# Performance work log

Hardware: AMD Instinct MI355X
Metric: run time of the kernel (lower is better)

The kernel has to match this reference:

```python
import jax, jax.numpy as jnp
import numpy as np

EPS = 1e-3  # BatchNormalization epsilon


def setup_inputs() -> dict:
    key = jax.random.key(0)
    ks = jax.random.split(key, 8)
    B, H, W, C = 16, 128, 128, 128
    f = C // 2  # filters = max(1, C // 2)
    x = jax.random.normal(ks[0], (B, H, W, C), dtype=jnp.float32)
    s_in = 1.0 / np.sqrt(C)
    s_f = 1.0 / np.sqrt(f)
    return {
        "x": x,
        "Wg": jax.random.normal(ks[1], (C, f), dtype=jnp.float32) * s_in,
        "bg": jnp.zeros((f,), jnp.float32),
        "Wt": jax.random.normal(ks[2], (C, f), dtype=jnp.float32) * s_in,
        "bt": jnp.zeros((f,), jnp.float32),
        "Wp": jax.random.normal(ks[3], (C, f), dtype=jnp.float32) * s_in,
        "bp": jnp.zeros((f,), jnp.float32),
        "Wo": jax.random.normal(ks[4], (f, f), dtype=jnp.float32) * s_f,
        "bo": jnp.zeros((f,), jnp.float32),
        "gamma": jnp.ones((f,), jnp.float32),
        "beta": jnp.zeros((f,), jnp.float32),
        "moving_mean": jnp.zeros((f,), jnp.float32),
        "moving_var": jnp.ones((f,), jnp.float32),
    }


def reference(x, Wg, bg, Wt, bt, Wp, bp, Wo, bo, gamma, beta, moving_mean, moving_var):
    B, H, W, C = x.shape
    f = Wg.shape[1]
    N = H * W
    # 1x1 conv projections (NHWC): einsum over channel dim, then flatten spatial
    g = (jnp.einsum('bhwc,cf->bhwf', x, Wg) + bg).reshape(B, N, f)     # [B,N,f]
    tx = (jnp.einsum('bhwc,cf->bhwf', x, Wt) + bt).reshape(B, N, f)    # theta
    ty = (jnp.einsum('bhwc,cf->bhwf', x, Wp) + bp).reshape(B, N, f)    # phi
    # keras Dot(axes=[1,2]) on ([B,N,f], Permute->[B,f,N]) contracts the N axes
    # -> f x f Gram matrix per batch element.
    fm = jnp.einsum('bni,bnj->bij', tx, ty)                            # [B,f,f]
    fm = jax.nn.softmax(fm, axis=-1)
    # second Dot(axes=[1,2]): contract fm axis 1 (i) with g axis 2 (i) -> [B,f,N]
    z = jnp.einsum('bij,bni->bjn', fm, g)                              # [B,f,N]
    # Reshape flat-reinterprets [B, f*N] as [B,H,W,f]
    z = z.reshape(B, H, W, f)
    # output 1x1 conv (f -> f channels)
    z = jnp.einsum('bhwf,fe->bhwe', z, Wo) + bo
    # BatchNorm, inference mode (moving statistics)
    inv = gamma * jax.lax.rsqrt(moving_var + EPS)
    z = (z - moving_mean) * inv + beta
    return z
```

## Files before the change

kernel.cpp:

```cpp
#include <hip/hip_runtime.h>
#include <stdint.h>

#define B_ 16
#define H_ 128
#define W_ 128
#define C_ 128
#define F_ 64
#define N_ (H_*W_)
#define SPLITS 32
#define RPB (N_/SPLITS)
#define CH 64
#define EPSV 1e-3f

typedef __attribute__((ext_vector_type(8))) short bf16x8;
typedef __attribute__((ext_vector_type(16))) float f32x16;

__device__ __forceinline__ unsigned short f2b(float f) {
    unsigned int x = __float_as_uint(f);
    x += 0x7fffu + ((x >> 16) & 1u);
    return (unsigned short)(x >> 16);
}
__device__ __forceinline__ float b2f(unsigned short u) {
    return __uint_as_float(((unsigned int)u) << 16);
}

__global__ __launch_bounds__(256, 2)
void kS(const float* __restrict__ x, const float* __restrict__ Wg,
        const float* __restrict__ bg, unsigned short* __restrict__ g,
        float* __restrict__ Spart, float* __restrict__ cspart)
{
    __shared__ unsigned int  xsT_hi[C_][36];
    __shared__ unsigned int  xsT_lo[C_][36];
    __shared__ __align__(16) unsigned short xs_pool[CH][136];
    __shared__ __align__(16) unsigned short gT[CH][72];

    const int tid  = threadIdx.x;
    const int lane = tid & 63;
    const int w    = tid >> 6;
    const int b    = blockIdx.x >> 5;
    const int sp   = blockIdx.x & 31;

    const float* xb = x + ((size_t)b * N_ + (size_t)sp * RPB) * C_;
    unsigned short* gb = g + ((size_t)b * N_ + (size_t)sp * RPB) * F_;

    const int rowA = lane & 31;
    const int hiL  = lane >> 5;
    const int kgrp = hiL * 8;
    const int c1b  = (w & 1) * 64;
    const int c2b  = (w >> 1) * 64;
    const int nbG  = (w & 1) * 32;
    const int fbG  = (w >> 1) * 32;

    const float bgl = bg[fbG + rowA];

    for (int i = tid; i < C_*F_; i += 256) {
        int c = i >> 6, f = i & 63;
        xs_pool[f][c] = f2b(Wg[i]);
    }
    __syncthreads();
    bf16x8 wgfr[8];
    #pragma unroll
    for (int ks = 0; ks < 8; ++ks)
        wgfr[ks] = *(const bf16x8*)&xs_pool[fbG + rowA][ks*16 + kgrp];
    __syncthreads();

    f32x16 accS[2][2];
    #pragma unroll
    for (int ti = 0; ti < 2; ++ti)
        #pragma unroll
        for (int tj = 0; tj < 2; ++tj)
            #pragma unroll
            for (int e = 0; e < 16; ++e) accS[ti][tj][e] = 0.f;
    float csum = 0.f;

    const int sr = tid >> 2;
    const int sc = (tid & 3) * 16;

    for (int ch = 0; ch < RPB/CH; ++ch) {
        const float* xc = xb + (size_t)ch * CH * C_;
        #pragma unroll
        for (int p = 0; p < 4; ++p) {
            const int idx = tid + 256*p;
            const int np  = idx & 31;
            const int c4  = (idx >> 5) * 4;
            const float* r0 = xc + (size_t)(2*np) * C_ + c4;
            float4 a = *(const float4*)r0;
            float4 q = *(const float4*)(r0 + C_);
            unsigned short ha0 = f2b(a.x), ha1 = f2b(a.y), ha2 = f2b(a.z), ha3 = f2b(a.w);
            unsigned short hb0 = f2b(q.x), hb1 = f2b(q.y), hb2 = f2b(q.z), hb3 = f2b(q.w);
            unsigned short la0 = f2b(a.x - b2f(ha0)), la1 = f2b(a.y - b2f(ha1));
            unsigned short la2 = f2b(a.z - b2f(ha2)), la3 = f2b(a.w - b2f(ha3));
            unsigned short lb0 = f2b(q.x - b2f(hb0)), lb1 = f2b(q.y - b2f(hb1));
            unsigned short lb2 = f2b(q.z - b2f(hb2)), lb3 = f2b(q.w - b2f(hb3));
            if (p == 0) __syncthreads();
            xsT_hi[c4+0][np] = (unsigned)ha0 | ((unsigned)hb0 << 16);
            xsT_hi[c4+1][np] = (unsigned)ha1 | ((unsigned)hb1 << 16);
            xsT_hi[c4+2][np] = (unsigned)ha2 | ((unsigned)hb2 << 16);
            xsT_hi[c4+3][np] = (unsigned)ha3 | ((unsigned)hb3 << 16);
            xsT_lo[c4+0][np] = (unsigned)la0 | ((unsigned)lb0 << 16);
            xsT_lo[c4+1][np] = (unsigned)la1 | ((unsigned)lb1 << 16);
            xsT_lo[c4+2][np] = (unsigned)la2 | ((unsigned)lb2 << 16);
            xsT_lo[c4+3][np] = (unsigned)la3 | ((unsigned)lb3 << 16);
            ushort4 u0; u0.x = ha0; u0.y = ha1; u0.z = ha2; u0.w = ha3;
            ushort4 u1; u1.x = hb0; u1.y = hb1; u1.z = hb2; u1.w = hb3;
            *(ushort4*)&xs_pool[2*np  ][c4] = u0;
            *(ushort4*)&xs_pool[2*np+1][c4] = u1;
        }

        if (ch) {
            uint4 v0 = *(const uint4*)&gT[sr][sc];
            uint4 v1 = *(const uint4*)&gT[sr][sc + 8];
            unsigned short* dst = gb + (size_t)((ch-1)*CH + sr) * F_ + sc;
            *(uint4*)dst       = v0;
            *(uint4*)(dst + 8) = v1;
        }
        __syncthreads();

        if (tid < C_) {
            #pragma unroll 8
            for (int npp = 0; npp < 32; ++npp) {
                unsigned int h = xsT_hi[tid][npp];
                unsigned int l = xsT_lo[tid][npp];
                csum += b2f((unsigned short)(h & 0xffffu)) + b2f((unsigned short)(h >> 16))
                      + b2f((unsigned short)(l & 0xffffu)) + b2f((unsigned short)(l >> 16));
            }
        }

        {
            f32x16 aG;
            #pragma unroll
            for (int e = 0; e < 16; ++e) aG[e] = 0.f;
            #pragma unroll
            for (int ks = 0; ks < 8; ++ks) {
                bf16x8 av = *(const bf16x8*)&xs_pool[nbG + rowA][ks*16 + kgrp];
                aG = __builtin_amdgcn_mfma_f32_32x32x16_bf16(av, wgfr[ks], aG, 0, 0, 0);
            }
            const int fcol = fbG + rowA;
            #pragma unroll
            for (int r = 0; r < 16; ++r) {
                int nloc = (r & 3) + 8*(r >> 2) + 4*hiL;
                gT[nbG + nloc][fcol] = f2b(aG[r] + bgl);
            }
        }

        #pragma unroll
        for (int ks = 0; ks < 4; ++ks) {
            const int kn = ks*16 + kgrp;
            bf16x8 Ah[2], Al[2], Bh[2], Bl[2];
            #pragma unroll
            for (int t = 0; t < 2; ++t) {
                const unsigned short* rAh = (const unsigned short*)&xsT_hi[c1b + 32*t + rowA][0];
                const unsigned short* rAl = (const unsigned short*)&xsT_lo[c1b + 32*t + rowA][0];
                Ah[t] = *(const bf16x8*)(rAh + kn);
                Al[t] = *(const bf16x8*)(rAl + kn);
                const unsigned short* rBh = (const unsigned short*)&xsT_hi[c2b + 32*t + rowA][0];
                const unsigned short* rBl = (const unsigned short*)&xsT_lo[c2b + 32*t + rowA][0];
                Bh[t] = *(const bf16x8*)(rBh + kn);
                Bl[t] = *(const bf16x8*)(rBl + kn);
            }
            #pragma unroll
            for (int ti = 0; ti < 2; ++ti)
                #pragma unroll
                for (int tj = 0; tj < 2; ++tj) {
                    accS[ti][tj] = __builtin_amdgcn_mfma_f32_32x32x16_bf16(Ah[ti], Bh[tj], accS[ti][tj], 0, 0, 0);
                    accS[ti][tj] = __builtin_amdgcn_mfma_f32_32x32x16_bf16(Ah[ti], Bl[tj], accS[ti][tj], 0, 0, 0);
                    accS[ti][tj] = __builtin_amdgcn_mfma_f32_32x32x16_bf16(Al[ti], Bh[tj], accS[ti][tj], 0, 0, 0);
                }
        }
    }

    __syncthreads();
    {
        uint4 v0 = *(const uint4*)&gT[sr][sc];
        uint4 v1 = *(const uint4*)&gT[sr][sc + 8];
        unsigned short* dst = gb + (size_t)((RPB/CH - 1)*CH + sr) * F_ + sc;
        *(uint4*)dst       = v0;
        *(uint4*)(dst + 8) = v1;
    }

    float* so = Spart + (size_t)(b * SPLITS + sp) * (size_t)(C_ * C_);
    #pragma unroll
    for (int ti = 0; ti < 2; ++ti)
        #pragma unroll
        for (int tj = 0; tj < 2; ++tj)
            #pragma unroll
            for (int r = 0; r < 16; ++r) {
                int c1 = c1b + 32*ti + (r & 3) + 8*(r >> 2) + 4*hiL;
                int c2 = c2b + 32*tj + rowA;
                so[(size_t)c1 * C_ + c2] = accS[ti][tj][r];
            }
    if (tid < C_)
        cspart[(size_t)(b * SPLITS + sp) * C_ + tid] = csum;
}

__global__ __launch_bounds__(256, 8)
void kR(const float* __restrict__ Spart, const float* __restrict__ cspart,
        float* __restrict__ Sred, float* __restrict__ csred)
{
    const int b = blockIdx.x >> 4;
    const int r = blockIdx.x & 15;
    const int f4 = r*256 + threadIdx.x;
    const float4* base = (const float4*)(Spart + (size_t)b * SPLITS * C_ * C_);
    float sx=0.f, sy=0.f, sz=0.f, sw=0.f;
    #pragma unroll 4
    for (int sp = 0; sp < SPLITS; ++sp) {
        float4 v = base[(size_t)sp * (C_*C_/4) + f4];
        sx += v.x; sy += v.y; sz += v.z; sw += v.w;
    }
    ((float4*)(Sred + (size_t)b * C_ * C_))[f4] = make_float4(sx, sy, sz, sw);

    if (r == 0 && threadIdx.x < C_) {
        float c = 0.f;
        #pragma unroll 4
        for (int sp = 0; sp < SPLITS; ++sp)
            c += cspart[((size_t)b * SPLITS + sp) * C_ + threadIdx.x];
        csred[(size_t)b * C_ + threadIdx.x] = c;
    }
}

__global__ __launch_bounds__(256, 2)
void kT(const float* __restrict__ Sred, const float* __restrict__ csred,
        const float* __restrict__ Wp, float* __restrict__ T1buf,
        float* __restrict__ T2buf)
{
    __shared__ float Ss[32][C_];
    __shared__ float Wps[C_][F_];

    const int tid = threadIdx.x;
    const int b = blockIdx.x >> 2;
    const int q = blockIdx.x & 3;

    const float4* sg = (const float4*)(Sred + ((size_t)b * C_ + q*32) * C_);
    for (int t = tid; t < 32*C_/4; t += 256) ((float4*)Ss)[t] = sg[t];
    const float4* wg = (const float4*)Wp;
    for (int t = tid; t < C_*F_/4; t += 256) ((float4*)Wps)[t] = wg[t];
    __syncthreads();

    const int lane = tid & 63;
    const int w    = tid >> 6;

    float acc[8] = {0.f,0.f,0.f,0.f,0.f,0.f,0.f,0.f};
    #pragma unroll 2
    for (int k = 0; k < C_; k += 4) {
        float w0 = Wps[k+0][lane];
        float w1 = Wps[k+1][lane];
        float w2 = Wps[k+2][lane];
        float w3 = Wps[k+3][lane];
        #pragma unroll
        for (int cl = 0; cl < 8; ++cl) {
            float4 sv = *(const float4*)&Ss[w*8 + cl][k];
            float t = acc[cl];
            t = fmaf(sv.x, w0, t);
            t = fmaf(sv.y, w1, t);
            t = fmaf(sv.z, w2, t);
            t = fmaf(sv.w, w3, t);
            acc[cl] = t;
        }
    }
    #pragma unroll
    for (int cl = 0; cl < 8; ++cl) {
        int c = q*32 + w*8 + cl;
        T1buf[((size_t)b * C_ + c) * F_ + lane] = acc[cl];
    }

    if (q == 0 && tid < F_) {
        const float* cv = csred + (size_t)b * C_;
        float s = 0.f;
        for (int k = 0; k < C_; ++k) s = fmaf(cv[k], Wps[k][tid], s);
        T2buf[(size_t)b * F_ + tid] = s;
    }
}

__global__ __launch_bounds__(256, 2)
void kF(const float* __restrict__ T1buf, const float* __restrict__ T2buf,
        const float* __restrict__ csred, const float* __restrict__ Wt,
        const float* __restrict__ bt, const float* __restrict__ bp,
        float* __restrict__ U)
{
    __shared__ float T1s[C_][F_];
    __shared__ float Wts[C_][F_];
    __shared__ float csb[C_];
    __shared__ float T2s[F_], T3s[F_], bts[F_], bps[F_];

    const int tid = threadIdx.x;
    const int b = blockIdx.x;

    for (int t = tid; t < C_*F_/4; t += 256) {
        ((float4*)T1s)[t] = ((const float4*)(T1buf + (size_t)b * C_ * F_))[t];
        ((float4*)Wts)[t] = ((const float4*)Wt)[t];
    }
    if (tid < C_) csb[tid] = csred[(size_t)b * C_ + tid];
    if (tid < F_) {
        T2s[tid] = T2buf[(size_t)b * F_ + tid];
        bts[tid] = bt[tid];
        bps[tid] = bp[tid];
    }
    __syncthreads();

    if (tid < F_) {
        float s = 0.f;
        for (int c = 0; c < C_; ++c) s = fmaf(csb[c], Wts[c][tid], s);
        T3s[tid] = s;
    }
    __syncthreads();

    const int lane = tid & 63;
    const int w    = tid >> 6;

    float acc[16];
    #pragma unroll
    for (int r = 0; r < 16; ++r) acc[r] = 0.f;

    #pragma unroll 2
    for (int c = 0; c < C_; ++c) {
        float t1 = T1s[c][lane];
        #pragma unroll
        for (int u = 0; u < 4; ++u) {
            float4 wv = *(const float4*)&Wts[c][w*16 + u*4];
            acc[u*4+0] = fmaf(wv.x, t1, acc[u*4+0]);
            acc[u*4+1] = fmaf(wv.y, t1, acc[u*4+1]);
            acc[u*4+2] = fmaf(wv.z, t1, acc[u*4+2]);
            acc[u*4+3] = fmaf(wv.w, t1, acc[u*4+3]);
        }
    }

    const float bpj = bps[lane];
    const float t2j = T2s[lane];
    #pragma unroll
    for (int r = 0; r < 16; ++r) {
        const int i = w*16 + r;
        float v = acc[r] + T3s[i]*bpj + bts[i]*(t2j + (float)N_ * bpj);
        float m = v;
        #pragma unroll
        for (int o = 32; o; o >>= 1) m = fmaxf(m, __shfl_xor(m, o));
        float e = expf(v - m);
        float s = e;
        #pragma unroll
        for (int o = 32; o; o >>= 1) s += __shfl_xor(s, o);
        U[((size_t)b * F_ + i) * F_ + lane] = e / s;
    }
}

__global__ __launch_bounds__(256, 2)
void kC(const unsigned short* __restrict__ g, const float* __restrict__ U,
        const float* __restrict__ Wo, const float* __restrict__ bo,
        const float* __restrict__ gamma_, const float* __restrict__ beta_,
        const float* __restrict__ mmean, const float* __restrict__ mvar,
        float* __restrict__ out)
{
    __shared__ __align__(16) unsigned short UT[F_][72];
    __shared__ __align__(16) unsigned short WoT[F_][72];
    __shared__ __align__(16) unsigned short M1T[4][32][72];

    const int tid  = threadIdx.x;
    const int lane = tid & 63;
    const int wv   = tid >> 6;
    const int jt   = wv & 1;
    const int et   = wv >> 1;

    const int wgrp = blockIdx.x & 15;
    const int half = (blockIdx.x >> 4) & 1;
    const int b    = blockIdx.x >> 5;

    for (int t = tid; t < 1024; t += 256) {
        const int i  = t >> 4;
        const int j4 = (t & 15) * 4;
        float4 uv = *(const float4*)(U + ((size_t)b * F_ + i) * F_ + j4);
        UT[j4+0][i] = f2b(uv.x); UT[j4+1][i] = f2b(uv.y);
        UT[j4+2][i] = f2b(uv.z); UT[j4+3][i] = f2b(uv.w);
        float4 wo4 = *(const float4*)(Wo + (size_t)i * F_ + j4);
        WoT[j4+0][i] = f2b(wo4.x); WoT[j4+1][i] = f2b(wo4.y);
        WoT[j4+2][i] = f2b(wo4.z); WoT[j4+3][i] = f2b(wo4.w);
    }
    __syncthreads();

    const int rowA = lane & 31;
    const int hi   = lane >> 5;
    const int hi8  = hi * 8;

    bf16x8 Ufr[4], WoFr[4];
    #pragma unroll
    for (int ks = 0; ks < 4; ++ks) {
        Ufr[ks]  = *(const bf16x8*)&UT [32*jt + rowA][16*ks + hi8];
        WoFr[ks] = *(const bf16x8*)&WoT[32*et + rowA][16*ks + hi8];
    }

    const int ep = 32*et + rowA;
    const float scl = gamma_[ep] * rsqrtf(mvar[ep] + EPSV);
    const float sft = (bo[ep] - mmean[ep]) * scl + beta_[ep];

    const unsigned short* gB = g + ((size_t)b * N_ + (size_t)half * (N_/2)) * F_;
    float* outB = out + (((size_t)b * H_ + half) * W_) * F_ + ep;
    const int w0 = wgrp * 8;

    unsigned short* m1row = &M1T[wv][rowA][0];

    auto gload = [&](bf16x8 (&D)[2][4], int widx) {
        const unsigned short* gw = gB + (size_t)widx * (64*F_) + (size_t)rowA * F_ + hi8;
        #pragma unroll
        for (int ft = 0; ft < 2; ++ft)
            #pragma unroll
            for (int ks = 0; ks < 4; ++ks)
                D[ft][ks] = *(const bf16x8*)(gw + ft*(32*F_) + 16*ks);
    };

    auto body = [&](bf16x8 (&G)[2][4], int widx) {
        f32x16 m0, m1, a2r;
        #pragma unroll
        for (int e = 0; e < 16; ++e) { m0[e] = 0.f; m1[e] = 0.f; a2r[e] = 0.f; }
        #pragma unroll
        for (int ks = 0; ks < 4; ++ks) {
            m0 = __builtin_amdgcn_mfma_f32_32x32x16_bf16(G[0][ks], Ufr[ks], m0, 0, 0, 0);
            m1 = __builtin_amdgcn_mfma_f32_32x32x16_bf16(G[1][ks], Ufr[ks], m1, 0, 0, 0);
        }
        #pragma unroll
        for (int r = 0; r < 16; r += 2) {
            const int e0 = (r & 3) + 8*(r >> 2) + 4*hi;
            const unsigned pw0 = (unsigned)f2b(m0[r]) | ((unsigned)f2b(m0[r+1]) << 16);
            *(unsigned int*)(m1row + e0) = pw0;
            const unsigned pw1 = (unsigned)f2b(m1[r]) | ((unsigned)f2b(m1[r+1]) << 16);
            *(unsigned int*)(m1row + 32 + e0) = pw1;
        }
        __syncthreads();
        #pragma unroll
        for (int ksg = 0; ksg < 4; ++ksg) {
            bf16x8 af = *(const bf16x8*)(m1row + 16*ksg + hi8);
            a2r = __builtin_amdgcn_mfma_f32_32x32x16_bf16(af, WoFr[ksg], a2r, 0, 0, 0);
        }
        float* ow = outB + (size_t)widx * F_ + (size_t)(64*jt + 8*hi) * (W_*F_);
        #pragma unroll
        for (int r = 0; r < 16; ++r) {
            const int off2j = 2*(r & 3) + 16*(r >> 2);
            ow[(size_t)off2j * (W_*F_)] = a2r[r] * scl + sft;
        }
        __syncthreads();
    };

    bf16x8 GA[2][4], GBf[2][4];
    gload(GA, w0);
    #pragma unroll
    for (int wi = 0; wi < 8; ++wi) {
        if (wi & 1) {
            if (wi < 7) gload(GA, w0 + wi + 1);
            body(GBf, w0 + wi);
        } else {
            if (wi < 7) gload(GBf, w0 + wi + 1);
            body(GA, w0 + wi);
        }
    }
}

extern "C" void kernel_launch(void* const* d_in, const int* in_sizes, int n_in,
                              void* d_out, int out_size, void* d_ws, size_t ws_size,
                              hipStream_t stream)
{
    const float* x  = (const float*)d_in[0];
    const float* Wg = (const float*)d_in[1];
    const float* bg = (const float*)d_in[2];
    const float* Wt = (const float*)d_in[3];
    const float* bt = (const float*)d_in[4];
    const float* Wp = (const float*)d_in[5];
    const float* bp = (const float*)d_in[6];
    const float* Wo = (const float*)d_in[7];
    const float* bo = (const float*)d_in[8];
    const float* ga = (const float*)d_in[9];
    const float* be = (const float*)d_in[10];
    const float* mm = (const float*)d_in[11];
    const float* mv = (const float*)d_in[12];
    float* out = (float*)d_out;

    char* ws = (char*)d_ws;
    unsigned short* g = (unsigned short*)ws;
    size_t off = (size_t)B_ * N_ * F_ * sizeof(unsigned short);
    float* Spart = (float*)(ws + off);
    float* T1buf = (float*)(ws + off);
    off += (size_t)B_ * SPLITS * C_ * C_ * sizeof(float);
    float* cspart = (float*)(ws + off);
    off += (size_t)B_ * SPLITS * C_ * sizeof(float);
    float* U = (float*)(ws + off);
    off += (size_t)B_ * F_ * F_ * sizeof(float);
    float* Sred = (float*)(ws + off);
    off += (size_t)B_ * C_ * C_ * sizeof(float);
    float* csred = (float*)(ws + off);
    off += (size_t)B_ * C_ * sizeof(float);
    float* T2buf = (float*)(ws + off);

    kS<<<B_ * SPLITS, 256, 0, stream>>>(x, Wg, bg, g, Spart, cspart);
    kR<<<B_ * 16, 256, 0, stream>>>(Spart, cspart, Sred, csred);
    kT<<<B_ * 4, 256, 0, stream>>>(Sred, csred, Wp, T1buf, T2buf);
    kF<<<B_, 256, 0, stream>>>(T1buf, T2buf, csred, Wt, bt, bp, U);
    kC<<<B_ * 2 * (W_/8), 256, 0, stream>>>(g, U, Wo, bo, ga, be, mm, mv, out);
}
```

Measured before the change: 110.2 us.

## Double kS block to 512 threads and split Gram tiles across eight waves

```diff
diff --git a/kernel.cpp b/kernel.cpp
--- a/kernel.cpp
+++ b/kernel.cpp
@@ -24,7 +24,7 @@
     return __uint_as_float(((unsigned int)u) << 16);
 }
 
-__global__ __launch_bounds__(256, 2)
+__global__ __launch_bounds__(512, 2)
 void kS(const float* __restrict__ x, const float* __restrict__ Wg,
         const float* __restrict__ bg, unsigned short* __restrict__ g,
         float* __restrict__ Spart, float* __restrict__ cspart)
@@ -36,7 +36,7 @@
 
     const int tid  = threadIdx.x;
     const int lane = tid & 63;
-    const int w    = tid >> 6;
+    const int v    = tid >> 6;
     const int b    = blockIdx.x >> 5;
     const int sp   = blockIdx.x & 31;
 
@@ -46,41 +46,40 @@
     const int rowA = lane & 31;
     const int hiL  = lane >> 5;
     const int kgrp = hiL * 8;
-    const int c1b  = (w & 1) * 64;
-    const int c2b  = (w >> 1) * 64;
-    const int nbG  = (w & 1) * 32;
-    const int fbG  = (w >> 1) * 32;
-
-    const float bgl = bg[fbG + rowA];
-
-    for (int i = tid; i < C_*F_; i += 256) {
+    const int rb   = v >> 1;
+    const int cbB  = (v & 1) * 64;
+    const int nbG  = (v & 1) * 32;
+    const int fbG  = (v >> 1) * 32;
+
+    const float bgl = (v < 4) ? bg[fbG + rowA] : 0.f;
+
+    for (int i = tid; i < C_*F_; i += 512) {
         int c = i >> 6, f = i & 63;
         xs_pool[f][c] = f2b(Wg[i]);
     }
     __syncthreads();
     bf16x8 wgfr[8];
-    #pragma unroll
-    for (int ks = 0; ks < 8; ++ks)
-        wgfr[ks] = *(const bf16x8*)&xs_pool[fbG + rowA][ks*16 + kgrp];
-    __syncthreads();
-
-    f32x16 accS[2][2];
-    #pragma unroll
-    for (int ti = 0; ti < 2; ++ti)
-        #pragma unroll
-        for (int tj = 0; tj < 2; ++tj)
-            #pragma unroll
-            for (int e = 0; e < 16; ++e) accS[ti][tj][e] = 0.f;
+    if (v < 4) {
+        #pragma unroll
+        for (int ks = 0; ks < 8; ++ks)
+            wgfr[ks] = *(const bf16x8*)&xs_pool[fbG + rowA][ks*16 + kgrp];
+    }
+
+    f32x16 accS[2];
+    #pragma unroll
+    for (int t = 0; t < 2; ++t)
+        #pragma unroll
+        for (int e = 0; e < 16; ++e) accS[t][e] = 0.f;
     float csum = 0.f;
 
-    const int sr = tid >> 2;
-    const int sc = (tid & 3) * 16;
+    const int sr = tid >> 3;
+    const int sc = (tid & 7) * 8;
 
     for (int ch = 0; ch < RPB/CH; ++ch) {
         const float* xc = xb + (size_t)ch * CH * C_;
         #pragma unroll
-        for (int p = 0; p < 4; ++p) {
-            const int idx = tid + 256*p;
+        for (int p = 0; p < 2; ++p) {
+            const int idx = tid + 512*p;
             const int np  = idx & 31;
             const int c4  = (idx >> 5) * 4;
             const float* r0 = xc + (size_t)(2*np) * C_ + c4;
@@ -107,26 +106,26 @@
             *(ushort4*)&xs_pool[2*np+1][c4] = u1;
         }
 
+        uint4 gv;
+        if (ch) gv = *(const uint4*)&gT[sr][sc];
+        __syncthreads();
         if (ch) {
-            uint4 v0 = *(const uint4*)&gT[sr][sc];
-            uint4 v1 = *(const uint4*)&gT[sr][sc + 8];
             unsigned short* dst = gb + (size_t)((ch-1)*CH + sr) * F_ + sc;
-            *(uint4*)dst       = v0;
-            *(uint4*)(dst + 8) = v1;
-        }
-        __syncthreads();
-
-        if (tid < C_) {
+            *(uint4*)dst = gv;
+        }
+
+        if (tid >= 256 && tid < 384) {
+            const int c = tid - 256;
             #pragma unroll 8
             for (int npp = 0; npp < 32; ++npp) {
-                unsigned int h = xsT_hi[tid][npp];
-                unsigned int l = xsT_lo[tid][npp];
+                unsigned int h = xsT_hi[c][npp];
+                unsigned int l = xsT_lo[c][npp];
                 csum += b2f((unsigned short)(h & 0xffffu)) + b2f((unsigned short)(h >> 16))
                       + b2f((unsigned short)(l & 0xffffu)) + b2f((unsigned short)(l >> 16));
             }
         }
 
-        {
+        if (v < 4) {
             f32x16 aG;
             #pragma unroll
             for (int e = 0; e < 16; ++e) aG[e] = 0.f;
@@ -146,51 +145,41 @@
         #pragma unroll
         for (int ks = 0; ks < 4; ++ks) {
             const int kn = ks*16 + kgrp;
-            bf16x8 Ah[2], Al[2], Bh[2], Bl[2];
+            bf16x8 Ah, Al, Bh[2], Bl[2];
+            Ah = *(const bf16x8*)((const unsigned short*)&xsT_hi[rb*32 + rowA][0] + kn);
+            Al = *(const bf16x8*)((const unsigned short*)&xsT_lo[rb*32 + rowA][0] + kn);
             #pragma unroll
             for (int t = 0; t < 2; ++t) {
-                const unsigned short* rAh = (const unsigned short*)&xsT_hi[c1b + 32*t + rowA][0];
-                const unsigned short* rAl = (const unsigned short*)&xsT_lo[c1b + 32*t + rowA][0];
-                Ah[t] = *(const bf16x8*)(rAh + kn);
-                Al[t] = *(const bf16x8*)(rAl + kn);
-                const unsigned short* rBh = (const unsigned short*)&xsT_hi[c2b + 32*t + rowA][0];
-                const unsigned short* rBl = (const unsigned short*)&xsT_lo[c2b + 32*t + rowA][0];
-                Bh[t] = *(const bf16x8*)(rBh + kn);
-                Bl[t] = *(const bf16x8*)(rBl + kn);
+                Bh[t] = *(const bf16x8*)((const unsigned short*)&xsT_hi[cbB + 32*t + rowA][0] + kn);
+                Bl[t] = *(const bf16x8*)((const unsigned short*)&xsT_lo[cbB + 32*t + rowA][0] + kn);
             }
             #pragma unroll
-            for (int ti = 0; ti < 2; ++ti)
-                #pragma unroll
-                for (int tj = 0; tj < 2; ++tj) {
-                    accS[ti][tj] = __builtin_amdgcn_mfma_f32_32x32x16_bf16(Ah[ti], Bh[tj], accS[ti][tj], 0, 0, 0);
-                    accS[ti][tj] = __builtin_amdgcn_mfma_f32_32x32x16_bf16(Ah[ti], Bl[tj], accS[ti][tj], 0, 0, 0);
-                    accS[ti][tj] = __builtin_amdgcn_mfma_f32_32x32x16_bf16(Al[ti], Bh[tj], accS[ti][tj], 0, 0, 0);
-                }
+            for (int t = 0; t < 2; ++t) {
+                accS[t] = __builtin_amdgcn_mfma_f32_32x32x16_bf16(Ah, Bh[t], accS[t], 0, 0, 0);
+                accS[t] = __builtin_amdgcn_mfma_f32_32x32x16_bf16(Ah, Bl[t], accS[t], 0, 0, 0);
+                accS[t] = __builtin_amdgcn_mfma_f32_32x32x16_bf16(Al, Bh[t], accS[t], 0, 0, 0);
+            }
         }
     }
 
     __syncthreads();
     {
-        uint4 v0 = *(const uint4*)&gT[sr][sc];
-        uint4 v1 = *(const uint4*)&gT[sr][sc + 8];
+        uint4 gv = *(const uint4*)&gT[sr][sc];
         unsigned short* dst = gb + (size_t)((RPB/CH - 1)*CH + sr) * F_ + sc;
-        *(uint4*)dst       = v0;
-        *(uint4*)(dst + 8) = v1;
+        *(uint4*)dst = gv;
     }
 
     float* so = Spart + (size_t)(b * SPLITS + sp) * (size_t)(C_ * C_);
     #pragma unroll
-    for (int ti = 0; ti < 2; ++ti)
-        #pragma unroll
-        for (int tj = 0; tj < 2; ++tj)
-            #pragma unroll
-            for (int r = 0; r < 16; ++r) {
-                int c1 = c1b + 32*ti + (r & 3) + 8*(r >> 2) + 4*hiL;
-                int c2 = c2b + 32*tj + rowA;
-                so[(size_t)c1 * C_ + c2] = accS[ti][tj][r];
-            }
-    if (tid < C_)
-        cspart[(size_t)(b * SPLITS + sp) * C_ + tid] = csum;
+    for (int t = 0; t < 2; ++t)
+        #pragma unroll
+        for (int r = 0; r < 16; ++r) {
+            int c1 = rb*32 + (r & 3) + 8*(r >> 2) + 4*hiL;
+            int c2 = cbB + 32*t + rowA;
+            so[(size_t)c1 * C_ + c2] = accS[t][r];
+        }
+    if (tid >= 256 && tid < 384)
+        cspart[(size_t)(b * SPLITS + sp) * C_ + (tid - 256)] = csum;
 }
 
 __global__ __launch_bounds__(256, 8)
@@ -485,7 +474,7 @@
     off += (size_t)B_ * C_ * sizeof(float);
     float* T2buf = (float*)(ws + off);
 
-    kS<<<B_ * SPLITS, 256, 0, stream>>>(x, Wg, bg, g, Spart, cspart);
+    kS<<<B_ * SPLITS, 512, 0, stream>>>(x, Wg, bg, g, Spart, cspart);
     kR<<<B_ * 16, 256, 0, stream>>>(Spart, cspart, Sred, csred);
     kT<<<B_ * 4, 256, 0, stream>>>(Sred, csred, Wp, T1buf, T2buf);
     kF<<<B_, 256, 0, stream>>>(T1buf, T2buf, csred, Wt, bt, bp, U);
```

Measured after the change: 133.1 us. +20.9%, slower.

## Double-buffer shared memory in kS and prefetch next x chunk into registers

Applied to the files above, without the earlier changes.

```diff
diff --git a/kernel.cpp b/kernel.cpp
--- a/kernel.cpp
+++ b/kernel.cpp
@@ -10,6 +10,7 @@
 #define SPLITS 32
 #define RPB (N_/SPLITS)
 #define CH 64
+#define NCH (RPB/CH)
 #define EPSV 1e-3f
 
 typedef __attribute__((ext_vector_type(8))) short bf16x8;
@@ -24,15 +25,15 @@
     return __uint_as_float(((unsigned int)u) << 16);
 }
 
-__global__ __launch_bounds__(256, 2)
+__global__ __launch_bounds__(256, 1)
 void kS(const float* __restrict__ x, const float* __restrict__ Wg,
         const float* __restrict__ bg, unsigned short* __restrict__ g,
         float* __restrict__ Spart, float* __restrict__ cspart)
 {
-    __shared__ unsigned int  xsT_hi[C_][36];
-    __shared__ unsigned int  xsT_lo[C_][36];
-    __shared__ __align__(16) unsigned short xs_pool[CH][136];
-    __shared__ __align__(16) unsigned short gT[CH][72];
+    __shared__ unsigned int  xsT_hi[2][C_][36];
+    __shared__ unsigned int  xsT_lo[2][C_][36];
+    __shared__ __align__(16) unsigned short xs_pool[2][CH][136];
+    __shared__ __align__(16) unsigned short gT[2][CH][72];
 
     const int tid  = threadIdx.x;
     const int lane = tid & 63;
@@ -55,13 +56,13 @@
 
     for (int i = tid; i < C_*F_; i += 256) {
         int c = i >> 6, f = i & 63;
-        xs_pool[f][c] = f2b(Wg[i]);
+        xs_pool[0][f][c] = f2b(Wg[i]);
     }
     __syncthreads();
     bf16x8 wgfr[8];
     #pragma unroll
     for (int ks = 0; ks < 8; ++ks)
-        wgfr[ks] = *(const bf16x8*)&xs_pool[fbG + rowA][ks*16 + kgrp];
+        wgfr[ks] = *(const bf16x8*)&xs_pool[0][fbG + rowA][ks*16 + kgrp];
     __syncthreads();
 
     f32x16 accS[2][2];
@@ -76,7 +77,9 @@
     const int sr = tid >> 2;
     const int sc = (tid & 3) * 16;
 
-    for (int ch = 0; ch < RPB/CH; ++ch) {
+    float4 ra[4], rq[4];
+
+    auto loadChunk = [&](int ch) {
         const float* xc = xb + (size_t)ch * CH * C_;
         #pragma unroll
         for (int p = 0; p < 4; ++p) {
@@ -84,77 +87,81 @@
             const int np  = idx & 31;
             const int c4  = (idx >> 5) * 4;
             const float* r0 = xc + (size_t)(2*np) * C_ + c4;
-            float4 a = *(const float4*)r0;
-            float4 q = *(const float4*)(r0 + C_);
+            ra[p] = *(const float4*)r0;
+            rq[p] = *(const float4*)(r0 + C_);
+        }
+    };
+
+    auto convertStore = [&](int par) {
+        #pragma unroll
+        for (int p = 0; p < 4; ++p) {
+            const int idx = tid + 256*p;
+            const int np  = idx & 31;
+            const int c4  = (idx >> 5) * 4;
+            float4 a = ra[p], q = rq[p];
             unsigned short ha0 = f2b(a.x), ha1 = f2b(a.y), ha2 = f2b(a.z), ha3 = f2b(a.w);
             unsigned short hb0 = f2b(q.x), hb1 = f2b(q.y), hb2 = f2b(q.z), hb3 = f2b(q.w);
             unsigned short la0 = f2b(a.x - b2f(ha0)), la1 = f2b(a.y - b2f(ha1));
             unsigned short la2 = f2b(a.z - b2f(ha2)), la3 = f2b(a.w - b2f(ha3));
             unsigned short lb0 = f2b(q.x - b2f(hb0)), lb1 = f2b(q.y - b2f(hb1));
             unsigned short lb2 = f2b(q.z - b2f(hb2)), lb3 = f2b(q.w - b2f(hb3));
-            if (p == 0) __syncthreads();
-            xsT_hi[c4+0][np] = (unsigned)ha0 | ((unsigned)hb0 << 16);
-            xsT_hi[c4+1][np] = (unsigned)ha1 | ((unsigned)hb1 << 16);
-            xsT_hi[c4+2][np] = (unsigned)ha2 | ((unsigned)hb2 << 16);
-            xsT_hi[c4+3][np] = (unsigned)ha3 | ((unsigned)hb3 << 16);
-            xsT_lo[c4+0][np] = (unsigned)la0 | ((unsigned)lb0 << 16);
-            xsT_lo[c4+1][np] = (unsigned)la1 | ((unsigned)lb1 << 16);
-            xsT_lo[c4+2][np] = (unsigned)la2 | ((unsigned)lb2 << 16);
-            xsT_lo[c4+3][np] = (unsigned)la3 | ((unsigned)lb3 << 16);
+            xsT_hi[par][c4+0][np] = (unsigned)ha0 | ((unsigned)hb0 << 16);
+            xsT_hi[par][c4+1][np] = (unsigned)ha1 | ((unsigned)hb1 << 16);
+            xsT_hi[par][c4+2][np] = (unsigned)ha2 | ((unsigned)hb2 << 16);
+            xsT_hi[par][c4+3][np] = (unsigned)ha3 | ((unsigned)hb3 << 16);
+            xsT_lo[par][c4+0][np] = (unsigned)la0 | ((unsigned)lb0 << 16);
+            xsT_lo[par][c4+1][np] = (unsigned)la1 | ((unsigned)lb1 << 16);
+            xsT_lo[par][c4+2][np] = (unsigned)la2 | ((unsigned)lb2 << 16);
+            xsT_lo[par][c4+3][np] = (unsigned)la3 | ((unsigned)lb3 << 16);
             ushort4 u0; u0.x = ha0; u0.y = ha1; u0.z = ha2; u0.w = ha3;
             ushort4 u1; u1.x = hb0; u1.y = hb1; u1.z = hb2; u1.w = hb3;
-            *(ushort4*)&xs_pool[2*np  ][c4] = u0;
-            *(ushort4*)&xs_pool[2*np+1][c4] = u1;
-        }
-
-        if (ch) {
-            uint4 v0 = *(const uint4*)&gT[sr][sc];
-            uint4 v1 = *(const uint4*)&gT[sr][sc + 8];
-            unsigned short* dst = gb + (size_t)((ch-1)*CH + sr) * F_ + sc;
-            *(uint4*)dst       = v0;
-            *(uint4*)(dst + 8) = v1;
-        }
-        __syncthreads();
-
+            *(ushort4*)&xs_pool[par][2*np  ][c4] = u0;
+            *(ushort4*)&xs_pool[par][2*np+1][c4] = u1;
+        }
+    };
+
+    auto csumPhase = [&](int par) {
         if (tid < C_) {
             #pragma unroll 8
             for (int npp = 0; npp < 32; ++npp) {
-                unsigned int h = xsT_hi[tid][npp];
-                unsigned int l = xsT_lo[tid][npp];
+                unsigned int h = xsT_hi[par][tid][npp];
+                unsigned int l = xsT_lo[par][tid][npp];
                 csum += b2f((unsigned short)(h & 0xffffu)) + b2f((unsigned short)(h >> 16))
                       + b2f((unsigned short)(l & 0xffffu)) + b2f((unsigned short)(l >> 16));
             }
         }
-
-        {
-            f32x16 aG;
-            #pragma unroll
-            for (int e = 0; e < 16; ++e) aG[e] = 0.f;
-            #pragma unroll
-            for (int ks = 0; ks < 8; ++ks) {
-                bf16x8 av = *(const bf16x8*)&xs_pool[nbG + rowA][ks*16 + kgrp];
-                aG = __builtin_amdgcn_mfma_f32_32x32x16_bf16(av, wgfr[ks], aG, 0, 0, 0);
-            }
-            const int fcol = fbG + rowA;
-            #pragma unroll
-            for (int r = 0; r < 16; ++r) {
-                int nloc = (r & 3) + 8*(r >> 2) + 4*hiL;
-                gT[nbG + nloc][fcol] = f2b(aG[r] + bgl);
-            }
-        }
-
+    };
+
+    auto gPhase = [&](int par) {
+        f32x16 aG;
+        #pragma unroll
+        for (int e = 0; e < 16; ++e) aG[e] = 0.f;
+        #pragma unroll
+        for (int ks = 0; ks < 8; ++ks) {
+            bf16x8 av = *(const bf16x8*)&xs_pool[par][nbG + rowA][ks*16 + kgrp];
+            aG = __builtin_amdgcn_mfma_f32_32x32x16_bf16(av, wgfr[ks], aG, 0, 0, 0);
+        }
+        const int fcol = fbG + rowA;
+        #pragma unroll
+        for (int r = 0; r < 16; ++r) {
+            int nloc = (r & 3) + 8*(r >> 2) + 4*hiL;
+            gT[par][nbG + nloc][fcol] = f2b(aG[r] + bgl);
+        }
+    };
+
+    auto sPhase = [&](int par) {
         #pragma unroll
         for (int ks = 0; ks < 4; ++ks) {
             const int kn = ks*16 + kgrp;
             bf16x8 Ah[2], Al[2], Bh[2], Bl[2];
             #pragma unroll
             for (int t = 0; t < 2; ++t) {
-                const unsigned short* rAh = (const unsigned short*)&xsT_hi[c1b + 32*t + rowA][0];
-                const unsigned short* rAl = (const unsigned short*)&xsT_lo[c1b + 32*t + rowA][0];
+                const unsigned short* rAh = (const unsigned short*)&xsT_hi[par][c1b + 32*t + rowA][0];
+                const unsigned short* rAl = (const unsigned short*)&xsT_lo[par][c1b + 32*t + rowA][0];
                 Ah[t] = *(const bf16x8*)(rAh + kn);
                 Al[t] = *(const bf16x8*)(rAl + kn);
-                const unsigned short* rBh = (const unsigned short*)&xsT_hi[c2b + 32*t + rowA][0];
-                const unsigned short* rBl = (const unsigned short*)&xsT_lo[c2b + 32*t + rowA][0];
+                const unsigned short* rBh = (const unsigned short*)&xsT_hi[par][c2b + 32*t + rowA][0];
+                const unsigned short* rBl = (const unsigned short*)&xsT_lo[par][c2b + 32*t + rowA][0];
                 Bh[t] = *(const bf16x8*)(rBh + kn);
                 Bl[t] = *(const bf16x8*)(rBl + kn);
             }
@@ -167,15 +174,41 @@
                     accS[ti][tj] = __builtin_amdgcn_mfma_f32_32x32x16_bf16(Al[ti], Bh[tj], accS[ti][tj], 0, 0, 0);
                 }
         }
-    }
-
-    __syncthreads();
-    {
-        uint4 v0 = *(const uint4*)&gT[sr][sc];
-        uint4 v1 = *(const uint4*)&gT[sr][sc + 8];
-        unsigned short* dst = gb + (size_t)((RPB/CH - 1)*CH + sr) * F_ + sc;
+    };
+
+    auto gStore = [&](int par, int ch) {
+        uint4 v0 = *(const uint4*)&gT[par][sr][sc];
+        uint4 v1 = *(const uint4*)&gT[par][sr][sc + 8];
+        unsigned short* dst = gb + (size_t)(ch*CH + sr) * F_ + sc;
         *(uint4*)dst       = v0;
         *(uint4*)(dst + 8) = v1;
+    };
+
+    loadChunk(0);
+    convertStore(0);
+    loadChunk(1);
+    __syncthreads();
+
+    for (int i = 1; i < NCH; ++i) {
+        const int pc = (i - 1) & 1;
+        const int pw = i & 1;
+        if (i >= 2) gStore(pw, i - 2);
+        csumPhase(pc);
+        gPhase(pc);
+        sPhase(pc);
+        convertStore(pw);
+        if (i < NCH - 1) loadChunk(i + 1);
+        __syncthreads();
+    }
+
+    {
+        const int pc = (NCH - 1) & 1;
+        gStore(pc ^ 1, NCH - 2);
+        csumPhase(pc);
+        gPhase(pc);
+        sPhase(pc);
+        __syncthreads();
+        gStore(pc, NCH - 1);
     }
 
     float* so = Spart + (size_t)(b * SPLITS + sp) * (size_t)(C_ * C_);
```

New measurement: 123.9 us. +12.5%, slower.

## Prefetch x chunk into registers and compute channel sums with warp shuffles

Applied to the files above, without the earlier changes.

```diff
diff --git a/kernel.cpp b/kernel.cpp
--- a/kernel.cpp
+++ b/kernel.cpp
@@ -10,6 +10,7 @@
 #define SPLITS 32
 #define RPB (N_/SPLITS)
 #define CH 64
+#define NCH (RPB/CH)
 #define EPSV 1e-3f
 
 typedef __attribute__((ext_vector_type(8))) short bf16x8;
@@ -71,28 +72,50 @@
         for (int tj = 0; tj < 2; ++tj)
             #pragma unroll
             for (int e = 0; e < 16; ++e) accS[ti][tj][e] = 0.f;
-    float csum = 0.f;
+
+    float4 csr[4];
+    #pragma unroll
+    for (int p = 0; p < 4; ++p) csr[p] = make_float4(0.f, 0.f, 0.f, 0.f);
 
     const int sr = tid >> 2;
     const int sc = (tid & 3) * 16;
 
-    for (int ch = 0; ch < RPB/CH; ++ch) {
-        const float* xc = xb + (size_t)ch * CH * C_;
+    for (int ch = 0; ch < NCH; ++ch) {
+        __syncthreads();
+
+        float4 ra[4], rq[4];
+        {
+            const float* xc = xb + (size_t)ch * CH * C_;
+            #pragma unroll
+            for (int p = 0; p < 4; ++p) {
+                const int idx = tid + 256*p;
+                const float* r0 = xc + (size_t)(2*(idx & 31)) * C_ + ((idx >> 5) * 4);
+                ra[p] = *(const float4*)r0;
+                rq[p] = *(const float4*)(r0 + C_);
+            }
+        }
+        uint4 gv0, gv1;
+        if (ch) {
+            gv0 = *(const uint4*)&gT[sr][sc];
+            gv1 = *(const uint4*)&gT[sr][sc + 8];
+        }
+
         #pragma unroll
         for (int p = 0; p < 4; ++p) {
             const int idx = tid + 256*p;
             const int np  = idx & 31;
             const int c4  = (idx >> 5) * 4;
-            const float* r0 = xc + (size_t)(2*np) * C_ + c4;
-            float4 a = *(const float4*)r0;
-            float4 q = *(const float4*)(r0 + C_);
+            float4 a = ra[p], q = rq[p];
+            csr[p].x += a.x + q.x;
+            csr[p].y += a.y + q.y;
+            csr[p].z += a.z + q.z;
+            csr[p].w += a.w + q.w;
             unsigned short ha0 = f2b(a.x), ha1 = f2b(a.y), ha2 = f2b(a.z), ha3 = f2b(a.w);
             unsigned short hb0 = f2b(q.x), hb1 = f2b(q.y), hb2 = f2b(q.z), hb3 = f2b(q.w);
             unsigned short la0 = f2b(a.x - b2f(ha0)), la1 = f2b(a.y - b2f(ha1));
             unsigned short la2 = f2b(a.z - b2f(ha2)), la3 = f2b(a.w - b2f(ha3));
             unsigned short lb0 = f2b(q.x - b2f(hb0)), lb1 = f2b(q.y - b2f(hb1));
             unsigned short lb2 = f2b(q.z - b2f(hb2)), lb3 = f2b(q.w - b2f(hb3));
-            if (p == 0) __syncthreads();
             xsT_hi[c4+0][np] = (unsigned)ha0 | ((unsigned)hb0 << 16);
             xsT_hi[c4+1][np] = (unsigned)ha1 | ((unsigned)hb1 << 16);
             xsT_hi[c4+2][np] = (unsigned)ha2 | ((unsigned)hb2 << 16);
@@ -108,23 +131,11 @@
         }
 
         if (ch) {
-            uint4 v0 = *(const uint4*)&gT[sr][sc];
-            uint4 v1 = *(const uint4*)&gT[sr][sc + 8];
             unsigned short* dst = gb + (size_t)((ch-1)*CH + sr) * F_ + sc;
-            *(uint4*)dst       = v0;
-            *(uint4*)(dst + 8) = v1;
+            *(uint4*)dst       = gv0;
+            *(uint4*)(dst + 8) = gv1;
         }
         __syncthreads();
-
-        if (tid < C_) {
-            #pragma unroll 8
-            for (int npp = 0; npp < 32; ++npp) {
-                unsigned int h = xsT_hi[tid][npp];
-                unsigned int l = xsT_lo[tid][npp];
-                csum += b2f((unsigned short)(h & 0xffffu)) + b2f((unsigned short)(h >> 16))
-                      + b2f((unsigned short)(l & 0xffffu)) + b2f((unsigned short)(l >> 16));
-            }
-        }
 
         {
             f32x16 aG;
@@ -171,11 +182,11 @@
 
     __syncthreads();
     {
-        uint4 v0 = *(const uint4*)&gT[sr][sc];
-        uint4 v1 = *(const uint4*)&gT[sr][sc + 8];
-        unsigned short* dst = gb + (size_t)((RPB/CH - 1)*CH + sr) * F_ + sc;
-        *(uint4*)dst       = v0;
-        *(uint4*)(dst + 8) = v1;
+        uint4 gv0 = *(const uint4*)&gT[sr][sc];
+        uint4 gv1 = *(const uint4*)&gT[sr][sc + 8];
+        unsigned short* dst = gb + (size_t)((NCH - 1)*CH + sr) * F_ + sc;
+        *(uint4*)dst       = gv0;
+        *(uint4*)(dst + 8) = gv1;
     }
 
     float* so = Spart + (size_t)(b * SPLITS + sp) * (size_t)(C_ * C_);
@@ -189,8 +200,29 @@
                 int c2 = c2b + 32*tj + rowA;
                 so[(size_t)c1 * C_ + c2] = accS[ti][tj][r];
             }
-    if (tid < C_)
-        cspart[(size_t)(b * SPLITS + sp) * C_ + tid] = csum;
+
+    #pragma unroll
+    for (int p = 0; p < 4; ++p) {
+        #pragma unroll
+        for (int o = 16; o; o >>= 1) {
+            csr[p].x += __shfl_xor(csr[p].x, o);
+            csr[p].y += __shfl_xor(csr[p].y, o);
+            csr[p].z += __shfl_xor(csr[p].z, o);
+            csr[p].w += __shfl_xor(csr[p].w, o);
+        }
+    }
+    if ((lane & 31) == 0) {
+        const int h = lane >> 5;
+        float* co = cspart + (size_t)(b * SPLITS + sp) * C_;
+        #pragma unroll
+        for (int p = 0; p < 4; ++p) {
+            const int c4 = 4 * (2*w + h + 8*p);
+            co[c4+0] = csr[p].x;
+            co[c4+1] = csr[p].y;
+            co[c4+2] = csr[p].z;
+            co[c4+3] = csr[p].w;
+        }
+    }
 }
 
 __global__ __launch_bounds__(256, 8)
```

New measurement: 107.4 us. -2.5%, faster.
